# Optimization experiments

Measured on AMD Instinct MI355X. Metric: run time of the kernel, lower is better.

Reference implementation:

```python
import jax, jax.numpy as jnp
import numpy as np

# Model dims
B, S, H, E, I, K = 2, 2048, 1024, 8, 1024, 2
ALPHA, LIMIT = 1.702, 7.0  # gpt_oss activation constants (module defaults)


def setup_inputs() -> dict:
    key = jax.random.key(0)
    ks = jax.random.split(key, 5)
    sc = 0.02
    return {
        "hidden_states": jax.random.normal(ks[0], (B, S, H), jnp.float32),
        "router_weight": jax.random.normal(ks[1], (H, E), jnp.float32) * sc,
        "gate_up_proj": jax.random.normal(ks[2], (E, H, 2 * I), jnp.float32) * sc,
        "gate_up_proj_bias": jnp.zeros((E, 2 * I), jnp.float32),
        "down_proj": jax.random.normal(ks[3], (E, I, H), jnp.float32) * sc,
        "down_proj_bias": jnp.zeros((E, H), jnp.float32),
    }


def reference(hidden_states, router_weight, gate_up_proj, gate_up_proj_bias,
              down_proj, down_proj_bias):
    Bt, St, Ht = hidden_states.shape
    x = hidden_states.reshape(-1, Ht)           # [T, H], T = B*S
    T = x.shape[0]

    # Router: linear -> top-k -> softmax over selected logits (gpt_oss style)
    logits = x @ router_weight                  # [T, E]
    top_vals, top_idx = jax.lax.top_k(logits, K)
    scores = jax.nn.softmax(top_vals, axis=-1)  # [T, K]
    # Sparse combine weights: w[t, e] = score if e selected for t, else 0
    w = jnp.zeros((T, E), x.dtype).at[jnp.arange(T)[:, None], top_idx].set(scores)

    # Fused gate+up projection for every expert (dense equivalent of grouped GEMM;
    # unselected experts get zero combine weight so math matches sparse path)
    gu = jnp.einsum('th,ehf->tef', x, gate_up_proj) + gate_up_proj_bias  # [T, E, 2I]
    gate = gu[..., ::2]                         # interleaved gate (default)
    up = gu[..., 1::2]
    gate = jnp.minimum(gate, LIMIT)
    up = jnp.clip(up, -LIMIT, LIMIT)
    glu = gate * jax.nn.sigmoid(gate * ALPHA)
    act = (up + 1.0) * glu                      # [T, E, I]

    down = jnp.einsum('tei,eih->teh', act, down_proj) + down_proj_bias  # [T, E, H]

    # Weighted combine over experts (all-to-all combine is identity at D=1)
    out = jnp.einsum('te,teh->th', w, down)     # [T, H]
    return out.reshape(Bt, St, Ht)
```

## Files before the change

### kernel.cpp

```cpp
#include <hip/hip_runtime.h>
#include <hip/hip_bf16.h>
#include <cstdint>
#include <cstddef>

constexpr int T_TOK = 4096;
constexpr int H_DIM = 1024;
constexpr int E_NUM = 8;
constexpr int I_DIM = 1024;
constexpr int F2    = 2048;
constexpr float ALPHA = 1.702f;
constexpr float LIMIT = 7.0f;
constexpr int BM = 256;
constexpr int BK = 32;
constexpr int NT = 32;
constexpr int MAXT = 40;

using u16    = unsigned short;
using bf16x8 = __attribute__((ext_vector_type(8))) __bf16;
using s16x8  = __attribute__((ext_vector_type(8))) short;
using f32x4  = __attribute__((ext_vector_type(4))) float;

constexpr size_t WS_W1T  = 0;
constexpr size_t WS_DOWN = 0;
constexpr size_t WS_W2T  = 33554432;
constexpr size_t WS_ACT  = 50331648;
constexpr size_t WS_ETOK = 67108864;
constexpr size_t WS_POS  = 67239936;
constexpr size_t WS_CNT  = 67272704;
constexpr size_t WS_ROWB = 67272736;
constexpr size_t WS_ASGN = 67272768;
constexpr size_t WS_TOPE = 67273792;
constexpr size_t WS_TOPW = 67290176;
constexpr size_t WS_XBF  = 67322944;
constexpr size_t WS_NEED = 75711552;

__device__ __forceinline__ u16 f2bf(float f) {
    union { float f; unsigned u; } v; v.f = f;
    return (u16)((v.u + 0x7FFFu + ((v.u >> 16) & 1u)) >> 16);
}
__device__ __forceinline__ float bf2f(u16 u) {
    union { unsigned u; float f; } v; v.u = (unsigned)u << 16; return v.f;
}

__device__ __forceinline__ s16x8 pack8(float4 a, float4 b) {
    s16x8 r;
    r[0] = (short)f2bf(a.x); r[1] = (short)f2bf(a.y);
    r[2] = (short)f2bf(a.z); r[3] = (short)f2bf(a.w);
    r[4] = (short)f2bf(b.x); r[5] = (short)f2bf(b.y);
    r[6] = (short)f2bf(b.z); r[7] = (short)f2bf(b.w);
    return r;
}

__device__ __forceinline__ void gload16(const void* g, void* l) {
    __builtin_amdgcn_global_load_lds((const __attribute__((address_space(1))) unsigned*)g,
                                     (__attribute__((address_space(3))) unsigned*)l,
                                     16, 0, 0);
}

__device__ __forceinline__ void pipe_sync() {
    __builtin_amdgcn_sched_barrier(0);
    asm volatile("s_waitcnt vmcnt(0) lgkmcnt(0)" ::: "memory");
    __builtin_amdgcn_s_barrier();
    __builtin_amdgcn_sched_barrier(0);
}

__global__ __launch_bounds__(256) void k_xbf(const float* __restrict__ x,
                                             u16* __restrict__ xbf) {
    const size_t i = ((size_t)blockIdx.x * 256 + threadIdx.x) * 8;
    float4 a = *(const float4*)(x + i);
    float4 b = *(const float4*)(x + i + 4);
    *(s16x8*)(xbf + i) = pack8(a, b);
}

__global__ __launch_bounds__(256) void k_transpose_w1(const float* __restrict__ in,
                                                      u16* __restrict__ out) {
    __shared__ float tile[64][65];
    const int e = blockIdx.z, c0 = blockIdx.x * 64, h0 = blockIdx.y * 64;
    const int tid = threadIdx.x;
    const float* src = in + ((size_t)e * H_DIM + h0) * F2 + c0;
#pragma unroll
    for (int i = 0; i < 4; ++i) {
        int r = (tid >> 4) + i * 16, c = (tid & 15) * 4;
        float4 v = *(const float4*)(src + (size_t)r * F2 + c);
        tile[r][c] = v.x; tile[r][c + 1] = v.y; tile[r][c + 2] = v.z; tile[r][c + 3] = v.w;
    }
    __syncthreads();
    const int c = tid >> 2, hseg = (tid & 3) * 16;
    const int g = c & 1;
    const int f = (c0 + c) >> 1;
    u16* dst = out + (((size_t)e * 2 + g) * I_DIM + f) * H_DIM + h0 + hseg;
    s16x8 o0, o1;
#pragma unroll
    for (int j = 0; j < 8; ++j) o0[j] = (short)f2bf(tile[hseg + j][c]);
#pragma unroll
    for (int j = 0; j < 8; ++j) o1[j] = (short)f2bf(tile[hseg + 8 + j][c]);
    *(s16x8*)dst = o0;
    *(s16x8*)(dst + 8) = o1;
}

__global__ __launch_bounds__(256) void k_transpose_w2(const float* __restrict__ in,
                                                      u16* __restrict__ out) {
    __shared__ float tile[64][65];
    const int e = blockIdx.z, h0 = blockIdx.x * 64, i0 = blockIdx.y * 64;
    const int tid = threadIdx.x;
    const float* src = in + ((size_t)e * I_DIM + i0) * H_DIM + h0;
#pragma unroll
    for (int i = 0; i < 4; ++i) {
        int r = (tid >> 4) + i * 16, c = (tid & 15) * 4;
        float4 v = *(const float4*)(src + (size_t)r * H_DIM + c);
        tile[r][c] = v.x; tile[r][c + 1] = v.y; tile[r][c + 2] = v.z; tile[r][c + 3] = v.w;
    }
    __syncthreads();
    const int c = tid >> 2, iseg = (tid & 3) * 16;
    u16* dst = out + ((size_t)e * H_DIM + h0 + c) * I_DIM + i0 + iseg;
    s16x8 o0, o1;
#pragma unroll
    for (int j = 0; j < 8; ++j) o0[j] = (short)f2bf(tile[iseg + j][c]);
#pragma unroll
    for (int j = 0; j < 8; ++j) o1[j] = (short)f2bf(tile[iseg + 8 + j][c]);
    *(s16x8*)dst = o0;
    *(s16x8*)(dst + 8) = o1;
}

__global__ __launch_bounds__(256) void k_router_top2(const float* __restrict__ x,
                                                     const float* __restrict__ rw,
                                                     int* __restrict__ tope,
                                                     float2* __restrict__ topw) {
    const int wave = threadIdx.x >> 6, lane = threadIdx.x & 63;
    const int t = blockIdx.x * 4 + wave;
    const float* xr = x + (size_t)t * H_DIM;
    float acc[E_NUM];
#pragma unroll
    for (int e = 0; e < E_NUM; ++e) acc[e] = 0.f;
    for (int h = lane; h < H_DIM; h += 64) {
        float xv = xr[h];
        const float* r = rw + h * E_NUM;
#pragma unroll
        for (int e = 0; e < E_NUM; ++e) acc[e] += xv * r[e];
    }
#pragma unroll
    for (int e = 0; e < E_NUM; ++e) {
        float v = acc[e];
#pragma unroll
        for (int o = 32; o > 0; o >>= 1) v += __shfl_down(v, o);
        acc[e] = v;
    }
    if (lane == 0) {
        int e0 = 0; float v0 = acc[0];
#pragma unroll
        for (int e = 1; e < E_NUM; ++e) if (acc[e] > v0) { v0 = acc[e]; e0 = e; }
        int e1 = -1; float v1 = -3.4e38f;
#pragma unroll
        for (int e = 0; e < E_NUM; ++e) if (e != e0 && acc[e] > v1) { v1 = acc[e]; e1 = e; }
        float ew = expf(v1 - v0);
        float inv = 1.f / (1.f + ew);
        tope[t] = e0 | (e1 << 8);
        topw[t] = make_float2(inv, ew * inv);
    }
}

__global__ __launch_bounds__(256) void k_router_scatter(const int* __restrict__ tope,
                                                        int* __restrict__ cnt,
                                                        int* __restrict__ ent_tok,
                                                        int2* __restrict__ pos) {
    __shared__ int lcnt[E_NUM];
    __shared__ int gbase[E_NUM];
    const int tid = threadIdx.x;
    const int t = blockIdx.x * 256 + tid;
    if (tid < E_NUM) lcnt[tid] = 0;
    __syncthreads();
    const int pk = tope[t];
    const int e0 = pk & 0xff, e1 = pk >> 8;
    const int o0 = atomicAdd(&lcnt[e0], 1);
    const int o1 = atomicAdd(&lcnt[e1], 1);
    __syncthreads();
    if (tid < E_NUM) gbase[tid] = atomicAdd(&cnt[tid], lcnt[tid]);
    __syncthreads();
    const int p0 = gbase[e0] + o0;
    const int p1 = gbase[e1] + o1;
    ent_tok[e0 * T_TOK + p0] = t;
    ent_tok[e1 * T_TOK + p1] = t;
    pos[t] = make_int2(p0, p1);
}

__global__ void k_schedule(const int* __restrict__ cnt, int* __restrict__ rowbase,
                           int* __restrict__ assign) {
    if (threadIdx.x == 0) {
        int rb = 0, na = 0;
        for (int e = 0; e < E_NUM; ++e) {
            rowbase[e] = rb;
            int nt = (cnt[e] + BM - 1) >> 8;
            for (int m = 0; m < nt; ++m) assign[na++] = (e << 16) | m;
            rb += cnt[e];
        }
        for (; na < MAXT; ++na) assign[na] = -1;
    }
}

__global__ __launch_bounds__(512, 4) void k_gemm1(
    const u16* __restrict__ xbf, const u16* __restrict__ w1t,
    const float* __restrict__ bias, const int* __restrict__ ent_tok,
    const int* __restrict__ cnt, const int* __restrict__ rowbase,
    const int* __restrict__ assign, u16* __restrict__ act) {
    const int a = assign[blockIdx.y];
    if (a < 0) return;
    const int e = a >> 16, mt = a & 0xffff;
    const int j0 = blockIdx.x * 64;
    const int cs = cnt[e], r0 = mt * BM;
    __shared__ __align__(16) u16 As[2][BM * BK];
    __shared__ __align__(16) u16 Bs[2][128 * BK];
    const int tid = threadIdx.x, lane = tid & 63, wv = tid >> 6;
    const int lr = lane >> 2;
    const int sm = (lane & 3) ^ ((lr >> 1) & 3);
    const u16* asrc[2]; int dofsA[2];
#pragma unroll
    for (int j = 0; j < 2; ++j) {
        const int row = wv * 32 + j * 16 + lr;
        const int aent = r0 + row;
        const int tok = (aent < cs) ? ent_tok[e * T_TOK + aent] : 0;
        asrc[j] = xbf + (size_t)tok * H_DIM + sm * 8;
        dofsA[j] = (wv * 32 + j * 16) * BK;
    }
    const int brow = wv * 16 + lr;
    const int bg = brow >> 6;
    const int bf = j0 + (brow & 63);
    const u16* bsrc = w1t + (((size_t)e * 2 + bg) * I_DIM + bf) * H_DIM + sm * 8;
    const int dofsB = (wv * 16) * BK;
    const int wm = wv >> 1, wn = wv & 1;
    const int lcol = lane & 15, lk = lane >> 4;
    int aoff[4], goff[2], uoff[2];
#pragma unroll
    for (int mi = 0; mi < 4; ++mi) {
        const int r = wm * 64 + mi * 16 + lcol;
        aoff[mi] = r * 64 + ((lk ^ ((r >> 1) & 3)) << 4);
    }
#pragma unroll
    for (int nj = 0; nj < 2; ++nj) {
        const int rg_ = wn * 32 + nj * 16 + lcol;
        const int ru  = 64 + rg_;
        goff[nj] = rg_ * 64 + ((lk ^ ((rg_ >> 1) & 3)) << 4);
        uoff[nj] = ru  * 64 + ((lk ^ ((ru  >> 1) & 3)) << 4);
    }
    f32x4 ag[4][2], au[4][2];
    const f32x4 z = {0.f, 0.f, 0.f, 0.f};
#pragma unroll
    for (int mi = 0; mi < 4; ++mi) { ag[mi][0] = z; ag[mi][1] = z; au[mi][0] = z; au[mi][1] = z; }
#pragma unroll
    for (int j = 0; j < 2; ++j) gload16(asrc[j], &As[0][dofsA[j]]);
    gload16(bsrc, &Bs[0][dofsB]);
    pipe_sync();
    int cur = 0;
    for (int t = 0; t < NT; ++t) {
        if (t + 1 < NT) {
            const int kn = (t + 1) * BK;
            u16* Ad = As[cur ^ 1]; u16* Bd = Bs[cur ^ 1];
#pragma unroll
            for (int j = 0; j < 2; ++j) gload16(asrc[j] + kn, Ad + dofsA[j]);
            gload16(bsrc + kn, Bd + dofsB);
        }
        const char* Ab = (const char*)As[cur];
        const char* Bb = (const char*)Bs[cur];
        bf16x8 af[4];
#pragma unroll
        for (int mi = 0; mi < 4; ++mi) af[mi] = *(const bf16x8*)(Ab + aoff[mi]);
        const bf16x8 g0 = *(const bf16x8*)(Bb + goff[0]);
        const bf16x8 g1 = *(const bf16x8*)(Bb + goff[1]);
        const bf16x8 u0 = *(const bf16x8*)(Bb + uoff[0]);
        const bf16x8 u1 = *(const bf16x8*)(Bb + uoff[1]);
#pragma unroll
        for (int mi = 0; mi < 4; ++mi) {
            ag[mi][0] = __builtin_amdgcn_mfma_f32_16x16x32_bf16(af[mi], g0, ag[mi][0], 0, 0, 0);
            au[mi][0] = __builtin_amdgcn_mfma_f32_16x16x32_bf16(af[mi], u0, au[mi][0], 0, 0, 0);
            ag[mi][1] = __builtin_amdgcn_mfma_f32_16x16x32_bf16(af[mi], g1, ag[mi][1], 0, 0, 0);
            au[mi][1] = __builtin_amdgcn_mfma_f32_16x16x32_bf16(af[mi], u1, au[mi][1], 0, 0, 0);
        }
        pipe_sync();
        cur ^= 1;
    }
    const int rbase = rowbase[e];
#pragma unroll
    for (int mi = 0; mi < 4; ++mi) {
#pragma unroll
        for (int nj = 0; nj < 2; ++nj) {
            const int col = j0 + wn * 32 + nj * 16 + lcol;
            const float bg_ = bias[e * F2 + 2 * col];
            const float bu_ = bias[e * F2 + 2 * col + 1];
#pragma unroll
            for (int rg = 0; rg < 4; ++rg) {
                const int r = wm * 64 + mi * 16 + lk * 4 + rg;
                if (r0 + r < cs) {
                    float gv = ag[mi][nj][rg] + bg_;
                    float uv = au[mi][nj][rg] + bu_;
                    gv = fminf(gv, LIMIT);
                    uv = fminf(fmaxf(uv, -LIMIT), LIMIT);
                    const float glu = gv / (1.f + expf(-ALPHA * gv));
                    act[(size_t)(rbase + r0 + r) * I_DIM + col] = f2bf((uv + 1.f) * glu);
                }
            }
        }
    }
}

__global__ __launch_bounds__(512, 4) void k_gemm2(
    const u16* __restrict__ actb, const u16* __restrict__ w2t,
    const int* __restrict__ cnt, const int* __restrict__ rowbase,
    const int* __restrict__ assign, u16* __restrict__ down) {
    const int a = assign[blockIdx.y];
    if (a < 0) return;
    const int e = a >> 16, mt = a & 0xffff;
    const int n0 = blockIdx.x * 128;
    const int cs = cnt[e], r0 = mt * BM, rbase = rowbase[e];
    __shared__ __align__(16) u16 As[2][BM * BK];
    __shared__ __align__(16) u16 Bs[2][128 * BK];
    const int tid = threadIdx.x, lane = tid & 63, wv = tid >> 6;
    const int lr = lane >> 2;
    const int sm = (lane & 3) ^ ((lr >> 1) & 3);
    const u16* asrc[2]; int dofsA[2];
#pragma unroll
    for (int j = 0; j < 2; ++j) {
        const int row = wv * 32 + j * 16 + lr;
        int ar = rbase + r0 + row;
        if (ar > 2 * T_TOK - 1) ar = 2 * T_TOK - 1;
        asrc[j] = actb + (size_t)ar * I_DIM + sm * 8;
        dofsA[j] = (wv * 32 + j * 16) * BK;
    }
    const int brow = wv * 16 + lr;
    const u16* bsrc = w2t + ((size_t)e * H_DIM + n0 + brow) * I_DIM + sm * 8;
    const int dofsB = (wv * 16) * BK;
    const int wm = wv >> 1, wn = wv & 1;
    const int lcol = lane & 15, lk = lane >> 4;
    int aoff[4], boff[4];
#pragma unroll
    for (int mi = 0; mi < 4; ++mi) {
        const int r = wm * 64 + mi * 16 + lcol;
        aoff[mi] = r * 64 + ((lk ^ ((r >> 1) & 3)) << 4);
    }
#pragma unroll
    for (int nj = 0; nj < 4; ++nj) {
        const int b = wn * 64 + nj * 16 + lcol;
        boff[nj] = b * 64 + ((lk ^ ((b >> 1) & 3)) << 4);
    }
    f32x4 acc[4][4];
    const f32x4 z = {0.f, 0.f, 0.f, 0.f};
#pragma unroll
    for (int mi = 0; mi < 4; ++mi)
#pragma unroll
        for (int nj = 0; nj < 4; ++nj) acc[mi][nj] = z;
#pragma unroll
    for (int j = 0; j < 2; ++j) gload16(asrc[j], &As[0][dofsA[j]]);
    gload16(bsrc, &Bs[0][dofsB]);
    pipe_sync();
    int cur = 0;
    for (int t = 0; t < NT; ++t) {
        if (t + 1 < NT) {
            const int kn = (t + 1) * BK;
            u16* Ad = As[cur ^ 1]; u16* Bd = Bs[cur ^ 1];
#pragma unroll
            for (int j = 0; j < 2; ++j) gload16(asrc[j] + kn, Ad + dofsA[j]);
            gload16(bsrc + kn, Bd + dofsB);
        }
        const char* Ab = (const char*)As[cur];
        const char* Bb = (const char*)Bs[cur];
        bf16x8 af[4], bf_[4];
#pragma unroll
        for (int mi = 0; mi < 4; ++mi) af[mi]  = *(const bf16x8*)(Ab + aoff[mi]);
#pragma unroll
        for (int nj = 0; nj < 4; ++nj) bf_[nj] = *(const bf16x8*)(Bb + boff[nj]);
#pragma unroll
        for (int mi = 0; mi < 4; ++mi)
#pragma unroll
            for (int nj = 0; nj < 4; ++nj)
                acc[mi][nj] = __builtin_amdgcn_mfma_f32_16x16x32_bf16(af[mi], bf_[nj], acc[mi][nj], 0, 0, 0);
        pipe_sync();
        cur ^= 1;
    }
#pragma unroll
    for (int mi = 0; mi < 4; ++mi) {
#pragma unroll
        for (int nj = 0; nj < 4; ++nj) {
            const int col = n0 + wn * 64 + nj * 16 + lcol;
#pragma unroll
            for (int rg = 0; rg < 4; ++rg) {
                const int r = wm * 64 + mi * 16 + lk * 4 + rg;
                if (r0 + r < cs)
                    down[(size_t)(rbase + r0 + r) * H_DIM + col] = f2bf(acc[mi][nj][rg]);
            }
        }
    }
}

__global__ __launch_bounds__(256) void k_combine(
    const int* __restrict__ tope, const float2* __restrict__ topw,
    const int2* __restrict__ pos, const int* __restrict__ rowb,
    const float* __restrict__ b2, const u16* __restrict__ down,
    float* __restrict__ out) {
    const int t = blockIdx.x;
    const int c = threadIdx.x * 4;
    const int pk = tope[t];
    const int e0 = pk & 0xff, e1 = pk >> 8;
    const int2 pp = pos[t];
    const float2 w = topw[t];
    const size_t ro0 = (size_t)(rowb[e0] + pp.x) * H_DIM;
    const size_t ro1 = (size_t)(rowb[e1] + pp.y) * H_DIM;
    ushort4 d0 = *(const ushort4*)(down + ro0 + c);
    ushort4 d1 = *(const ushort4*)(down + ro1 + c);
    float4 bb0 = *(const float4*)(b2 + e0 * H_DIM + c);
    float4 bb1 = *(const float4*)(b2 + e1 * H_DIM + c);
    float4 o;
    o.x = w.x * (bf2f(d0.x) + bb0.x) + w.y * (bf2f(d1.x) + bb1.x);
    o.y = w.x * (bf2f(d0.y) + bb0.y) + w.y * (bf2f(d1.y) + bb1.y);
    o.z = w.x * (bf2f(d0.z) + bb0.z) + w.y * (bf2f(d1.z) + bb1.z);
    o.w = w.x * (bf2f(d0.w) + bb0.w) + w.y * (bf2f(d1.w) + bb1.w);
    *(float4*)(out + (size_t)t * H_DIM + c) = o;
}

extern "C" void kernel_launch(void* const* d_in, const int* in_sizes, int n_in,
                              void* d_out, int out_size, void* d_ws, size_t ws_size,
                              hipStream_t stream) {
    const float* x   = (const float*)d_in[0];
    const float* rw  = (const float*)d_in[1];
    const float* w1  = (const float*)d_in[2];
    const float* b1  = (const float*)d_in[3];
    const float* w2  = (const float*)d_in[4];
    const float* b2  = (const float*)d_in[5];
    float* out = (float*)d_out;
    char* ws = (char*)d_ws;

    if (ws_size < WS_NEED) return;

    u16*    W1T  = (u16*)(ws + WS_W1T);
    u16*    DOWN = (u16*)(ws + WS_DOWN);
    u16*    W2T  = (u16*)(ws + WS_W2T);
    u16*    ACT  = (u16*)(ws + WS_ACT);
    int*    ETOK = (int*)(ws + WS_ETOK);
    int2*   POS  = (int2*)(ws + WS_POS);
    int*    CNT  = (int*)(ws + WS_CNT);
    int*    ROWB = (int*)(ws + WS_ROWB);
    int*    ASGN = (int*)(ws + WS_ASGN);
    int*    TOPE = (int*)(ws + WS_TOPE);
    float2* TOPW = (float2*)(ws + WS_TOPW);
    u16*    XBF  = (u16*)(ws + WS_XBF);

    hipMemsetAsync(CNT, 0, E_NUM * sizeof(int), stream);

    k_xbf<<<T_TOK * H_DIM / 2048, 256, 0, stream>>>(x, XBF);
    k_transpose_w1<<<dim3(32, 16, 8), 256, 0, stream>>>(w1, W1T);
    k_transpose_w2<<<dim3(16, 16, 8), 256, 0, stream>>>(w2, W2T);
    k_router_top2<<<T_TOK / 4, 256, 0, stream>>>(x, rw, TOPE, TOPW);
    k_router_scatter<<<T_TOK / 256, 256, 0, stream>>>(TOPE, CNT, ETOK, POS);
    k_schedule<<<1, 64, 0, stream>>>(CNT, ROWB, ASGN);
    k_gemm1<<<dim3(16, MAXT), 512, 0, stream>>>(XBF, W1T, b1, ETOK, CNT, ROWB, ASGN, ACT);
    k_gemm2<<<dim3(8, MAXT), 512, 0, stream>>>(ACT, W2T, CNT, ROWB, ASGN, DOWN);
    k_combine<<<T_TOK, 256, 0, stream>>>(TOPE, TOPW, POS, ROWB, b2, DOWN, out);
}
```

Measured before the change: 170.7 us.

## Pre-tile weights and activations into swizzled LDS-ready blocks for contiguous loads

Weight transpose kernels now write W1 and W2 as per-panel, per-k-tile contiguous blocks that already carry the XOR swizzle used in shared memory. The gemm1 epilogue writes activations in the same blocked, swizzled layout, with row bases padded to 256 so gemm2 can stream whole A tiles contiguously. The goal is to turn strided row loads into fully contiguous global-to-LDS copies with better coalescing. In exchange the activation workspace grows and the gemm1 epilogue does scattered 2-byte stores with more complex address arithmetic.

```diff
diff --git a/kernel.cpp b/kernel.cpp
--- a/kernel.cpp
+++ b/kernel.cpp
@@ -24,15 +24,15 @@
 constexpr size_t WS_DOWN = 0;
 constexpr size_t WS_W2T  = 33554432;
 constexpr size_t WS_ACT  = 50331648;
-constexpr size_t WS_ETOK = 67108864;
-constexpr size_t WS_POS  = 67239936;
-constexpr size_t WS_CNT  = 67272704;
-constexpr size_t WS_ROWB = 67272736;
-constexpr size_t WS_ASGN = 67272768;
-constexpr size_t WS_TOPE = 67273792;
-constexpr size_t WS_TOPW = 67290176;
-constexpr size_t WS_XBF  = 67322944;
-constexpr size_t WS_NEED = 75711552;
+constexpr size_t WS_ETOK = 71303168;
+constexpr size_t WS_POS  = 71434240;
+constexpr size_t WS_CNT  = 71467008;
+constexpr size_t WS_ROWB = 71467040;
+constexpr size_t WS_ASGN = 71467072;
+constexpr size_t WS_TOPE = 71468096;
+constexpr size_t WS_TOPW = 71484480;
+constexpr size_t WS_XBF  = 71517248;
+constexpr size_t WS_NEED = 79905856;
 
 __device__ __forceinline__ u16 f2bf(float f) {
     union { float f; unsigned u; } v; v.f = f;
@@ -88,14 +88,20 @@
     const int c = tid >> 2, hseg = (tid & 3) * 16;
     const int g = c & 1;
     const int f = (c0 + c) >> 1;
-    u16* dst = out + (((size_t)e * 2 + g) * I_DIM + f) * H_DIM + h0 + hseg;
     s16x8 o0, o1;
 #pragma unroll
     for (int j = 0; j < 8; ++j) o0[j] = (short)f2bf(tile[hseg + j][c]);
 #pragma unroll
     for (int j = 0; j < 8; ++j) o1[j] = (short)f2bf(tile[hseg + 8 + j][c]);
-    *(s16x8*)dst = o0;
-    *(s16x8*)(dst + 8) = o1;
+    const int pan = f >> 6;
+    const int brow = g * 64 + (f & 63);
+    const int h1 = h0 + hseg;
+    const int kt = h1 >> 5;
+    const int s0 = (h1 & 31) >> 3;
+    const int xr = (brow >> 1) & 3;
+    u16* blk = out + (((size_t)(e * 16 + pan) * 32 + kt) << 12);
+    *(s16x8*)(blk + brow * 32 + ((s0 ^ xr) << 3))       = o0;
+    *(s16x8*)(blk + brow * 32 + (((s0 + 1) ^ xr) << 3)) = o1;
 }
 
 __global__ __launch_bounds__(256) void k_transpose_w2(const float* __restrict__ in,
@@ -112,14 +118,21 @@
     }
     __syncthreads();
     const int c = tid >> 2, iseg = (tid & 3) * 16;
-    u16* dst = out + ((size_t)e * H_DIM + h0 + c) * I_DIM + i0 + iseg;
     s16x8 o0, o1;
 #pragma unroll
     for (int j = 0; j < 8; ++j) o0[j] = (short)f2bf(tile[iseg + j][c]);
 #pragma unroll
     for (int j = 0; j < 8; ++j) o1[j] = (short)f2bf(tile[iseg + 8 + j][c]);
-    *(s16x8*)dst = o0;
-    *(s16x8*)(dst + 8) = o1;
+    const int hcol = h0 + c;
+    const int pan = hcol >> 7;
+    const int brow = hcol & 127;
+    const int i1 = i0 + iseg;
+    const int kt = i1 >> 5;
+    const int s0 = (i1 & 31) >> 3;
+    const int xr = (brow >> 1) & 3;
+    u16* blk = out + (((size_t)(e * 8 + pan) * 32 + kt) << 12);
+    *(s16x8*)(blk + brow * 32 + ((s0 ^ xr) << 3))       = o0;
+    *(s16x8*)(blk + brow * 32 + (((s0 + 1) ^ xr) << 3)) = o1;
 }
 
 __global__ __launch_bounds__(256) void k_router_top2(const float* __restrict__ x,
@@ -192,6 +205,7 @@
             int nt = (cnt[e] + BM - 1) >> 8;
             for (int m = 0; m < nt; ++m) assign[na++] = (e << 16) | m;
             rb += cnt[e];
+            rb = (rb + 255) & ~255;
         }
         for (; na < MAXT; ++na) assign[na] = -1;
     }
@@ -205,7 +219,8 @@
     const int a = assign[blockIdx.y];
     if (a < 0) return;
     const int e = a >> 16, mt = a & 0xffff;
-    const int j0 = blockIdx.x * 64;
+    const int pan = blockIdx.x;
+    const int j0 = pan * 64;
     const int cs = cnt[e], r0 = mt * BM;
     __shared__ __align__(16) u16 As[2][BM * BK];
     __shared__ __align__(16) u16 Bs[2][128 * BK];
@@ -221,11 +236,8 @@
         asrc[j] = xbf + (size_t)tok * H_DIM + sm * 8;
         dofsA[j] = (wv * 32 + j * 16) * BK;
     }
-    const int brow = wv * 16 + lr;
-    const int bg = brow >> 6;
-    const int bf = j0 + (brow & 63);
-    const u16* bsrc = w1t + (((size_t)e * 2 + bg) * I_DIM + bf) * H_DIM + sm * 8;
-    const int dofsB = (wv * 16) * BK;
+    const u16* bblk = w1t + ((size_t)(e * 16 + pan) * 32) * 4096 + wv * 512 + lane * 8;
+    const int dofsB = wv * 512;
     const int wm = wv >> 1, wn = wv & 1;
     const int lcol = lane & 15, lk = lane >> 4;
     int aoff[4], goff[2], uoff[2];
@@ -247,7 +259,7 @@
     for (int mi = 0; mi < 4; ++mi) { ag[mi][0] = z; ag[mi][1] = z; au[mi][0] = z; au[mi][1] = z; }
 #pragma unroll
     for (int j = 0; j < 2; ++j) gload16(asrc[j], &As[0][dofsA[j]]);
-    gload16(bsrc, &Bs[0][dofsB]);
+    gload16(bblk, &Bs[0][dofsB]);
     pipe_sync();
     int cur = 0;
     for (int t = 0; t < NT; ++t) {
@@ -256,7 +268,7 @@
             u16* Ad = As[cur ^ 1]; u16* Bd = Bs[cur ^ 1];
 #pragma unroll
             for (int j = 0; j < 2; ++j) gload16(asrc[j] + kn, Ad + dofsA[j]);
-            gload16(bsrc + kn, Bd + dofsB);
+            gload16(bblk + (t + 1) * 4096, Bd + dofsB);
         }
         const char* Ab = (const char*)As[cur];
         const char* Bb = (const char*)Bs[cur];
@@ -285,6 +297,7 @@
             const int col = j0 + wn * 32 + nj * 16 + lcol;
             const float bg_ = bias[e * F2 + 2 * col];
             const float bu_ = bias[e * F2 + 2 * col + 1];
+            const int kt = col >> 5, slot = (col & 31) >> 3, ke = col & 7;
 #pragma unroll
             for (int rg = 0; rg < 4; ++rg) {
                 const int r = wm * 64 + mi * 16 + lk * 4 + rg;
@@ -294,7 +307,10 @@
                     gv = fminf(gv, LIMIT);
                     uv = fminf(fmaxf(uv, -LIMIT), LIMIT);
                     const float glu = gv / (1.f + expf(-ALPHA * gv));
-                    act[(size_t)(rbase + r0 + r) * I_DIM + col] = f2bf((uv + 1.f) * glu);
+                    const int grow = rbase + r0 + r;
+                    const int rr = grow & 255;
+                    act[((size_t)(grow >> 8) * 32 + kt) * 8192 + rr * 32 +
+                        ((slot ^ ((rr >> 1) & 3)) << 3) + ke] = f2bf((uv + 1.f) * glu);
                 }
             }
         }
@@ -308,25 +324,15 @@
     const int a = assign[blockIdx.y];
     if (a < 0) return;
     const int e = a >> 16, mt = a & 0xffff;
-    const int n0 = blockIdx.x * 128;
+    const int pan = blockIdx.x;
+    const int n0 = pan * 128;
     const int cs = cnt[e], r0 = mt * BM, rbase = rowbase[e];
     __shared__ __align__(16) u16 As[2][BM * BK];
     __shared__ __align__(16) u16 Bs[2][128 * BK];
     const int tid = threadIdx.x, lane = tid & 63, wv = tid >> 6;
-    const int lr = lane >> 2;
-    const int sm = (lane & 3) ^ ((lr >> 1) & 3);
-    const u16* asrc[2]; int dofsA[2];
-#pragma unroll
-    for (int j = 0; j < 2; ++j) {
-        const int row = wv * 32 + j * 16 + lr;
-        int ar = rbase + r0 + row;
-        if (ar > 2 * T_TOK - 1) ar = 2 * T_TOK - 1;
-        asrc[j] = actb + (size_t)ar * I_DIM + sm * 8;
-        dofsA[j] = (wv * 32 + j * 16) * BK;
-    }
-    const int brow = wv * 16 + lr;
-    const u16* bsrc = w2t + ((size_t)e * H_DIM + n0 + brow) * I_DIM + sm * 8;
-    const int dofsB = (wv * 16) * BK;
+    const u16* ablk = actb + ((size_t)((rbase + r0) >> 8) * 32) * 8192 + wv * 1024 + lane * 8;
+    const u16* bblk = w2t + ((size_t)(e * 8 + pan) * 32) * 4096 + wv * 512 + lane * 8;
+    const int dofsB = wv * 512;
     const int wm = wv >> 1, wn = wv & 1;
     const int lcol = lane & 15, lk = lane >> 4;
     int aoff[4], boff[4];
@@ -347,17 +353,17 @@
 #pragma unroll
         for (int nj = 0; nj < 4; ++nj) acc[mi][nj] = z;
 #pragma unroll
-    for (int j = 0; j < 2; ++j) gload16(asrc[j], &As[0][dofsA[j]]);
-    gload16(bsrc, &Bs[0][dofsB]);
+    for (int j = 0; j < 2; ++j) gload16(ablk + j * 512, &As[0][wv * 1024 + j * 512]);
+    gload16(bblk, &Bs[0][dofsB]);
     pipe_sync();
     int cur = 0;
     for (int t = 0; t < NT; ++t) {
         if (t + 1 < NT) {
-            const int kn = (t + 1) * BK;
             u16* Ad = As[cur ^ 1]; u16* Bd = Bs[cur ^ 1];
 #pragma unroll
-            for (int j = 0; j < 2; ++j) gload16(asrc[j] + kn, Ad + dofsA[j]);
-            gload16(bsrc + kn, Bd + dofsB);
+            for (int j = 0; j < 2; ++j)
+                gload16(ablk + (t + 1) * 8192 + j * 512, Ad + wv * 1024 + j * 512);
+            gload16(bblk + (t + 1) * 4096, Bd + dofsB);
         }
         const char* Ab = (const char*)As[cur];
         const char* Bb = (const char*)Bs[cur];
```

After: 163.4 us. 1.04x faster.
